# Optimization experiments

Hardware: AMD Instinct MI355X
Metric: run time of the kernel (lower is better)

Reference implementation:

```python
import jax, jax.numpy as jnp
import numpy as np

B, T, C, H = 4, 2048, 1024, 16
D = C // H  # head dim = 64

def setup_inputs() -> dict:
    key = jax.random.key(0)
    k1, k2, k3 = jax.random.split(key, 3)
    y = jax.random.normal(k1, (B, T, C), dtype=jnp.float32)
    W_attn = jax.random.normal(k2, (C, 3 * C), dtype=jnp.float32) * (1.0 / np.sqrt(C))
    b_attn = jnp.zeros((3 * C,), dtype=jnp.float32)
    W_proj = jax.random.normal(k3, (C, C), dtype=jnp.float32) * (1.0 / np.sqrt(C))
    b_proj = jnp.zeros((C,), dtype=jnp.float32)
    return {"y": y, "W_attn": W_attn, "b_attn": b_attn, "W_proj": W_proj, "b_proj": b_proj}

def reference(y, W_attn, b_attn, W_proj, b_proj):
    # qkv projection: [B,T,C] @ [C,3C] -> split into q,k,v
    qkv = y @ W_attn + b_attn
    q, k, v = jnp.split(qkv, 3, axis=-1)
    # [B,T,C] -> [B,H,T,D]
    q = q.reshape(B, T, H, D).swapaxes(1, 2)
    k = k.reshape(B, T, H, D).swapaxes(1, 2)
    v = v.reshape(B, T, H, D).swapaxes(1, 2)
    # scaled dot-product attention, non-causal (config default), dropout=0
    att = jnp.einsum('bhtd,bhrd->bhtr', q, k) * (1.0 / jnp.sqrt(jnp.float32(D)))
    att = jax.nn.softmax(att, axis=-1)
    out = jnp.einsum('bhts,bhsd->bhtd', att, v)
    out = out.swapaxes(1, 2).reshape(B, T, C)
    return out @ W_proj + b_proj
```

## Files before the change

### kernel.cpp

```cpp
#include <hip/hip_runtime.h>
#include <hip/hip_bf16.h>
#include <stdint.h>

#define B_ 4
#define T_ 2048
#define C_ 1024
#define H_ 16
#define D_ 64

typedef short bf16x8 __attribute__((ext_vector_type(8)));
typedef float f32x4 __attribute__((ext_vector_type(4)));
typedef unsigned short u16;

#define QSCALE 0.18033688011112042f

__device__ __forceinline__ u16 f2bf(float f) {
    __hip_bfloat16 h = __float2bfloat16(f);
    return *reinterpret_cast<u16*>(&h);
}

__device__ __forceinline__ float fexp2(float x) {
    float r;
    asm("v_exp_f32 %0, %1" : "=v"(r) : "v"(x));
    return r;
}

__device__ __forceinline__ void gload16(const void* g, void* l) {
    __builtin_amdgcn_global_load_lds(
        (const __attribute__((address_space(1))) unsigned int*)g,
        (__attribute__((address_space(3))) unsigned int*)l, 16, 0, 0);
}

__global__ void k_prep(const float* __restrict__ y, u16* __restrict__ y_bf,
                       const float* __restrict__ Wa, u16* __restrict__ WaT,
                       const float* __restrict__ Wp, u16* __restrict__ WpT) {
    const int bid = blockIdx.x, tid = threadIdx.x;
    if (bid < 8192) {
        int i = (bid * 256 + tid) * 4;
        float4 f = *reinterpret_cast<const float4*>(y + i);
        ushort4 o;
        o.x = f2bf(f.x); o.y = f2bf(f.y); o.z = f2bf(f.z); o.w = f2bf(f.w);
        *reinterpret_cast<ushort4*>(y_bf + i) = o;
        return;
    }
    __shared__ float tile[32][33];
    const float* src; u16* dst; int R, Cc, bx, by;
    if (bid < 8192 + 3072) {
        int idx = bid - 8192;
        src = Wa; dst = WaT; R = 1024; Cc = 3072;
        bx = idx % 96; by = idx / 96;
    } else {
        int idx = bid - 11264;
        src = Wp; dst = WpT; R = 1024; Cc = 1024;
        bx = idx & 31; by = idx >> 5;
    }
    int c0 = bx * 32, r0 = by * 32;
    int tx = tid & 31, ty = tid >> 5;
#pragma unroll
    for (int i = 0; i < 4; i++)
        tile[ty + i * 8][tx] = src[(size_t)(r0 + ty + i * 8) * Cc + c0 + tx];
    __syncthreads();
#pragma unroll
    for (int i = 0; i < 4; i++)
        dst[(size_t)(c0 + ty + i * 8) * R + r0 + tx] = f2bf(tile[tx][ty + i * 8]);
}

template <int EPI>
__launch_bounds__(256, 2)
__global__ void k_gemm(const u16* __restrict__ A, const u16* __restrict__ Bt,
                       const float* __restrict__ bias, int K, int N,
                       float* __restrict__ outf,
                       u16* __restrict__ qw, u16* __restrict__ kw, u16* __restrict__ vw) {
    __shared__ u16 As[128 * 64];
    __shared__ u16 Bs[128 * 64];
    const int tid = threadIdx.x;
    const int lane = tid & 63, w = tid >> 6;
    const int m0 = blockIdx.x * 128, n0 = blockIdx.y * 128;
    const int wm = (w >> 1) * 64, wn = (w & 1) * 64;
    const int lr = lane & 15, lg = lane >> 4;

    f32x4 acc[4][4];
#pragma unroll
    for (int i = 0; i < 4; i++)
#pragma unroll
        for (int j = 0; j < 4; j++) acc[i][j] = (f32x4){0.f, 0.f, 0.f, 0.f};

    const int nk = K >> 6;
    for (int kt = 0; kt < nk; ++kt) {
        const int k0 = kt * 64;
#pragma unroll
        for (int i = 0; i < 4; i++) {
            int c = i * 256 + tid;
            int row = c >> 3, k8 = (c & 7) << 3;
            gload16(A + (size_t)(m0 + row) * K + k0 + k8, (char*)As + i * 4096 + w * 1024);
            gload16(Bt + (size_t)(n0 + row) * K + k0 + k8, (char*)Bs + i * 4096 + w * 1024);
        }
        __syncthreads();
#pragma unroll
        for (int kk = 0; kk < 2; ++kk) {
            bf16x8 af[4], bfr[4];
#pragma unroll
            for (int mf = 0; mf < 4; ++mf)
                af[mf] = *reinterpret_cast<const bf16x8*>(&As[(wm + mf * 16 + lr) * 64 + kk * 32 + lg * 8]);
#pragma unroll
            for (int nf = 0; nf < 4; ++nf)
                bfr[nf] = *reinterpret_cast<const bf16x8*>(&Bs[(wn + nf * 16 + lr) * 64 + kk * 32 + lg * 8]);
#pragma unroll
            for (int mf = 0; mf < 4; ++mf)
#pragma unroll
                for (int nf = 0; nf < 4; ++nf)
                    acc[mf][nf] = __builtin_amdgcn_mfma_f32_16x16x32_bf16(af[mf], bfr[nf], acc[mf][nf], 0, 0, 0);
        }
        __syncthreads();
    }

    if (EPI == 0) {
#pragma unroll
        for (int mf = 0; mf < 4; ++mf)
#pragma unroll
            for (int nf = 0; nf < 4; ++nf) {
                int ng = n0 + wn + nf * 16 + lr;
                float bs = bias[ng];
#pragma unroll
                for (int r = 0; r < 4; ++r) {
                    int mg = m0 + wm + mf * 16 + lg * 4 + r;
                    outf[(size_t)mg * N + ng] = acc[mf][nf][r] + bs;
                }
            }
    } else {
        const int sec = n0 >> 10;
        const float sc = (sec == 0) ? QSCALE : 1.0f;
#pragma unroll
        for (int mf = 0; mf < 4; ++mf)
#pragma unroll
            for (int nf = 0; nf < 4; ++nf) {
                int ng = n0 + wn + nf * 16 + lr;
                float bs = bias[ng];
                int hd = ng & 1023;
                int h = hd >> 6, d = hd & 63;
                int mgb = m0 + wm + mf * 16 + lg * 4;
                int b = mgb >> 11, t0v = mgb & 2047;
                if (sec == 2) {
                    ushort4 pk;
                    pk.x = f2bf(acc[mf][nf][0] + bs);
                    pk.y = f2bf(acc[mf][nf][1] + bs);
                    pk.z = f2bf(acc[mf][nf][2] + bs);
                    pk.w = f2bf(acc[mf][nf][3] + bs);
                    *reinterpret_cast<ushort4*>(&vw[((size_t)(b * H_ + h) * D_ + d) * T_ + t0v]) = pk;
                } else {
                    u16* dst = (sec == 0) ? qw : kw;
#pragma unroll
                    for (int r = 0; r < 4; ++r)
                        dst[((size_t)(b * H_ + h) * T_ + t0v + r) * D_ + d] = f2bf((acc[mf][nf][r] + bs) * sc);
                }
            }
    }
}

__launch_bounds__(128, 2)
__global__ void k_attn(const u16* __restrict__ qw, const u16* __restrict__ kw,
                       const u16* __restrict__ vw, u16* __restrict__ attn) {
    __shared__ u16 Ks[2][64][64];
    __shared__ u16 Vs[2][64][64];
    const int tid = threadIdx.x, lane = tid & 63, w = tid >> 6;
    const int lr = lane & 15, lg = lane >> 4;
    const int bid = blockIdx.x;
    const int logical = (bid & 7) * 128 + (bid >> 3);
    const int bh = logical >> 4, qb = logical & 15;
    const int b = bh >> 4, h = bh & 15;
    const int q0 = qb * 128 + w * 64;
    const u16* qbase = qw + (size_t)bh * T_ * D_;
    const u16* kbase = kw + (size_t)bh * T_ * D_;
    const u16* vbase = vw + (size_t)bh * D_ * T_;

    bf16x8 qf[4][2];
#pragma unroll
    for (int jq = 0; jq < 4; jq++)
#pragma unroll
        for (int kd = 0; kd < 2; kd++)
            qf[jq][kd] = *reinterpret_cast<const bf16x8*>(
                &qbase[(size_t)(q0 + jq * 16 + lr) * D_ + kd * 32 + lg * 8]);

    auto stageK = [&](int kt, int buf) {
#pragma unroll
        for (int i = 0; i < 4; i++) {
            int idx = i * 128 + tid;
            int row = idx >> 3, ch = idx & 7;
            int gch = ch ^ ((row & 3) | (((row >> 3) & 1) << 2));
            gload16(kbase + ((size_t)(kt * 64 + row) * 64 + gch * 8),
                    (char*)&Ks[buf][0][0] + i * 2048 + w * 1024);
        }
    };
    auto stageV = [&](int kt, int buf) {
#pragma unroll
        for (int i = 0; i < 4; i++) {
            int idx = i * 128 + tid;
            int row = idx >> 3, ch = idx & 7;
            int gch = ch ^ (row & 7);
            gload16(vbase + ((size_t)row * T_ + kt * 64 + gch * 8),
                    (char*)&Vs[buf][0][0] + i * 2048 + w * 1024);
        }
    };

    f32x4 o[4][4];
#pragma unroll
    for (int md = 0; md < 4; md++)
#pragma unroll
        for (int jq = 0; jq < 4; jq++) o[md][jq] = (f32x4){0.f, 0.f, 0.f, 0.f};
    float l_run[4] = {0.f, 0.f, 0.f, 0.f};

    const int karow_base = ((lr >> 2) << 3) + (lr & 3);
    const int skl = ((lr & 3) | (((lr >> 2) & 1) << 2)) << 4;

    const int NT = T_ / 64;
    stageK(0, 0);
    stageV(0, 0);

    for (int kt = 0; kt < NT; ++kt) {
        const int cur = kt & 1;
        if (kt + 1 < NT) {
            stageK(kt + 1, cur ^ 1);
            stageV(kt + 1, cur ^ 1);
            asm volatile("s_waitcnt vmcnt(8)" ::: "memory");
        } else {
            asm volatile("s_waitcnt vmcnt(0)" ::: "memory");
        }
        __builtin_amdgcn_s_barrier();

        bf16x8 pfrag[4][2];
#pragma unroll
        for (int g = 0; g < 2; g++) {
            f32x4 st[2][4];
#pragma unroll
            for (int t = 0; t < 2; t++)
#pragma unroll
                for (int jq = 0; jq < 4; jq++) st[t][jq] = (f32x4){0.f, 0.f, 0.f, 0.f};
            __builtin_amdgcn_s_setprio(1);
#pragma unroll
            for (int t = 0; t < 2; t++) {
                int row = g * 32 + karow_base + t * 4;
#pragma unroll
                for (int kd = 0; kd < 2; kd++) {
                    bf16x8 ka = *reinterpret_cast<const bf16x8*>(
                        (const char*)&Ks[cur][0][0] + row * 128 + ((kd * 64 + lg * 16) ^ skl));
#pragma unroll
                    for (int jq = 0; jq < 4; jq++)
                        st[t][jq] = __builtin_amdgcn_mfma_f32_16x16x32_bf16(ka, qf[jq][kd], st[t][jq], 0, 0, 0);
                }
            }
            __builtin_amdgcn_s_setprio(0);
#pragma unroll
            for (int jq = 0; jq < 4; jq++) {
                float p0 = fexp2(st[0][jq][0]), p1 = fexp2(st[0][jq][1]);
                float p2 = fexp2(st[0][jq][2]), p3 = fexp2(st[0][jq][3]);
                float p4 = fexp2(st[1][jq][0]), p5 = fexp2(st[1][jq][1]);
                float p6 = fexp2(st[1][jq][2]), p7 = fexp2(st[1][jq][3]);
                l_run[jq] += ((p0 + p1) + (p2 + p3)) + ((p4 + p5) + (p6 + p7));
                pfrag[jq][g] = (bf16x8){(short)f2bf(p0), (short)f2bf(p1),
                                        (short)f2bf(p2), (short)f2bf(p3),
                                        (short)f2bf(p4), (short)f2bf(p5),
                                        (short)f2bf(p6), (short)f2bf(p7)};
            }
        }

#pragma unroll
        for (int g = 0; g < 2; g++) {
            bf16x8 va[4];
#pragma unroll
            for (int md = 0; md < 4; md++) {
                int row = md * 16 + lr;
                va[md] = *reinterpret_cast<const bf16x8*>(
                    (const char*)&Vs[cur][0][0] + row * 128 + ((g * 64 + lg * 16) ^ ((row & 7) << 4)));
            }
            __builtin_amdgcn_s_setprio(1);
#pragma unroll
            for (int md = 0; md < 4; md++)
#pragma unroll
                for (int jq = 0; jq < 4; jq++)
                    o[md][jq] = __builtin_amdgcn_mfma_f32_16x16x32_bf16(va[md], pfrag[jq][g], o[md][jq], 0, 0, 0);
            __builtin_amdgcn_s_setprio(0);
        }

        __builtin_amdgcn_s_barrier();
    }

#pragma unroll
    for (int jq = 0; jq < 4; jq++) {
        float l = l_run[jq];
        l += __shfl_xor(l, 16);
        l += __shfl_xor(l, 32);
        float rinv = 1.f / l;
        int q = q0 + jq * 16 + lr;
#pragma unroll
        for (int md = 0; md < 4; md++) {
            int d0 = md * 16 + lg * 4;
            ushort4 pk;
            pk.x = f2bf(o[md][jq][0] * rinv);
            pk.y = f2bf(o[md][jq][1] * rinv);
            pk.z = f2bf(o[md][jq][2] * rinv);
            pk.w = f2bf(o[md][jq][3] * rinv);
            *reinterpret_cast<ushort4*>(&attn[((size_t)(b * T_ + q)) * C_ + h * D_ + d0]) = pk;
        }
    }
}

extern "C" void kernel_launch(void* const* d_in, const int* in_sizes, int n_in,
                              void* d_out, int out_size, void* d_ws, size_t ws_size,
                              hipStream_t stream) {
    const float* y = (const float*)d_in[0];
    const float* W_attn = (const float*)d_in[1];
    const float* b_attn = (const float*)d_in[2];
    const float* W_proj = (const float*)d_in[3];
    const float* b_proj = (const float*)d_in[4];

    char* ws = (char*)d_ws;
    u16* y_bf = (u16*)(ws);
    u16* WaT  = (u16*)(ws + 16777216);
    u16* WpT  = (u16*)(ws + 16777216 + 6291456);
    u16* q_ws = (u16*)(ws + 25165824);
    u16* k_ws = (u16*)(ws + 25165824 + 16777216);
    u16* v_ws = (u16*)(ws + 25165824 + 33554432);
    u16* attn = (u16*)(ws + 25165824 + 50331648);

    k_prep<<<12288, 256, 0, stream>>>(y, y_bf, W_attn, WaT, W_proj, WpT);
    k_gemm<1><<<dim3(64, 24), 256, 0, stream>>>(y_bf, WaT, b_attn, 1024, 3072,
                                                nullptr, q_ws, k_ws, v_ws);
    k_attn<<<1024, 128, 0, stream>>>(q_ws, k_ws, v_ws, attn);
    k_gemm<0><<<dim3(64, 8), 256, 0, stream>>>(attn, WpT, b_proj, 1024, 1024,
                                               (float*)d_out, nullptr, nullptr, nullptr);
}
```

Measured before the change: 188.8 us.

## Software-pipeline attention across K tiles with 4 waves and triple-buffered V

Result: slower. 316.8 us (+67.8%).

```diff
diff --git a/kernel.cpp b/kernel.cpp
--- a/kernel.cpp
+++ b/kernel.cpp
@@ -157,135 +157,174 @@
     }
 }
 
-__launch_bounds__(128, 2)
+struct AttnCtx {
+    const char* Kb; const char* Vb;
+    const u16* kbase; const u16* vbase;
+    int tid, w, lr, lg, karow_base, skl;
+};
+
+__device__ __forceinline__ void a_stageK(const AttnCtx& c, int kt, int buf) {
+#pragma unroll
+    for (int i = 0; i < 2; i++) {
+        int idx = i * 256 + c.tid;
+        int row = idx >> 3, ch = idx & 7;
+        int gch = ch ^ ((row & 3) | (((row >> 3) & 1) << 2));
+        gload16(c.kbase + ((size_t)(kt * 64 + row) * 64 + gch * 8),
+                (char*)c.Kb + buf * 8192 + i * 4096 + c.w * 1024);
+    }
+}
+__device__ __forceinline__ void a_stageV(const AttnCtx& c, int kt, int vb) {
+#pragma unroll
+    for (int i = 0; i < 2; i++) {
+        int idx = i * 256 + c.tid;
+        int row = idx >> 3, ch = idx & 7;
+        int gch = ch ^ (row & 7);
+        gload16(c.vbase + ((size_t)row * T_ + kt * 64 + gch * 8),
+                (char*)c.Vb + vb * 8192 + i * 4096 + c.w * 1024);
+    }
+}
+
+template <bool FIRST, bool LAST>
+__device__ __forceinline__ void a_tile(const AttnCtx& c, int t, int curK,
+                                       int vb_cur, int vb_nxt, int vb_old,
+                                       const bf16x8 (&qf)[2][2],
+                                       bf16x8 (&pf_new)[2][2], const bf16x8 (&pf_old)[2][2],
+                                       f32x4 (&o)[4][2], float (&l_run)[2]) {
+    __builtin_amdgcn_s_barrier();
+    if (!LAST) {
+        a_stageK(c, t + 1, curK ^ 1);
+        a_stageV(c, t + 1, vb_nxt);
+        asm volatile("s_waitcnt vmcnt(4)" ::: "memory");
+    } else {
+        asm volatile("s_waitcnt vmcnt(0)" ::: "memory");
+    }
+    __builtin_amdgcn_s_barrier();
+
+    const char* Kc = c.Kb + curK * 8192;
+    const char* Vo = c.Vb + vb_old * 8192;
+#pragma unroll
+    for (int g = 0; g < 2; g++) {
+        f32x4 st[2][2];
+#pragma unroll
+        for (int t2 = 0; t2 < 2; t2++)
+#pragma unroll
+            for (int jq = 0; jq < 2; jq++) st[t2][jq] = (f32x4){0.f, 0.f, 0.f, 0.f};
+        __builtin_amdgcn_s_setprio(1);
+#pragma unroll
+        for (int t2 = 0; t2 < 2; t2++) {
+            int row = g * 32 + c.karow_base + t2 * 4;
+#pragma unroll
+            for (int kd = 0; kd < 2; kd++) {
+                bf16x8 ka = *reinterpret_cast<const bf16x8*>(
+                    Kc + row * 128 + ((kd * 64 + c.lg * 16) ^ c.skl));
+#pragma unroll
+                for (int jq = 0; jq < 2; jq++)
+                    st[t2][jq] = __builtin_amdgcn_mfma_f32_16x16x32_bf16(ka, qf[jq][kd], st[t2][jq], 0, 0, 0);
+            }
+        }
+        if (!FIRST) {
+#pragma unroll
+            for (int md = 0; md < 4; md++) {
+                int row = md * 16 + c.lr;
+                bf16x8 va = *reinterpret_cast<const bf16x8*>(
+                    Vo + row * 128 + ((g * 64 + c.lg * 16) ^ ((row & 7) << 4)));
+#pragma unroll
+                for (int jq = 0; jq < 2; jq++)
+                    o[md][jq] = __builtin_amdgcn_mfma_f32_16x16x32_bf16(va, pf_old[jq][g], o[md][jq], 0, 0, 0);
+            }
+        }
+        __builtin_amdgcn_s_setprio(0);
+#pragma unroll
+        for (int jq = 0; jq < 2; jq++) {
+            float p0 = fexp2(st[0][jq][0]), p1 = fexp2(st[0][jq][1]);
+            float p2 = fexp2(st[0][jq][2]), p3 = fexp2(st[0][jq][3]);
+            float p4 = fexp2(st[1][jq][0]), p5 = fexp2(st[1][jq][1]);
+            float p6 = fexp2(st[1][jq][2]), p7 = fexp2(st[1][jq][3]);
+            l_run[jq] += ((p0 + p1) + (p2 + p3)) + ((p4 + p5) + (p6 + p7));
+            pf_new[jq][g] = (bf16x8){(short)f2bf(p0), (short)f2bf(p1),
+                                     (short)f2bf(p2), (short)f2bf(p3),
+                                     (short)f2bf(p4), (short)f2bf(p5),
+                                     (short)f2bf(p6), (short)f2bf(p7)};
+        }
+    }
+}
+
+__launch_bounds__(256, 4)
 __global__ void k_attn(const u16* __restrict__ qw, const u16* __restrict__ kw,
                        const u16* __restrict__ vw, u16* __restrict__ attn) {
     __shared__ u16 Ks[2][64][64];
-    __shared__ u16 Vs[2][64][64];
+    __shared__ u16 Vs[3][64][64];
     const int tid = threadIdx.x, lane = tid & 63, w = tid >> 6;
     const int lr = lane & 15, lg = lane >> 4;
     const int bid = blockIdx.x;
     const int logical = (bid & 7) * 128 + (bid >> 3);
     const int bh = logical >> 4, qb = logical & 15;
     const int b = bh >> 4, h = bh & 15;
-    const int q0 = qb * 128 + w * 64;
+    const int q0 = qb * 128 + w * 32;
+
+    AttnCtx c;
+    c.Kb = (const char*)&Ks[0][0][0];
+    c.Vb = (const char*)&Vs[0][0][0];
+    c.kbase = kw + (size_t)bh * T_ * D_;
+    c.vbase = vw + (size_t)bh * D_ * T_;
+    c.tid = tid; c.w = w; c.lr = lr; c.lg = lg;
+    c.karow_base = ((lr >> 2) << 3) + (lr & 3);
+    c.skl = ((lr & 3) | (((lr >> 2) & 1) << 2)) << 4;
+
     const u16* qbase = qw + (size_t)bh * T_ * D_;
-    const u16* kbase = kw + (size_t)bh * T_ * D_;
-    const u16* vbase = vw + (size_t)bh * D_ * T_;
-
-    bf16x8 qf[4][2];
-#pragma unroll
-    for (int jq = 0; jq < 4; jq++)
+    bf16x8 qf[2][2];
+#pragma unroll
+    for (int jq = 0; jq < 2; jq++)
 #pragma unroll
         for (int kd = 0; kd < 2; kd++)
             qf[jq][kd] = *reinterpret_cast<const bf16x8*>(
                 &qbase[(size_t)(q0 + jq * 16 + lr) * D_ + kd * 32 + lg * 8]);
 
-    auto stageK = [&](int kt, int buf) {
-#pragma unroll
-        for (int i = 0; i < 4; i++) {
-            int idx = i * 128 + tid;
-            int row = idx >> 3, ch = idx & 7;
-            int gch = ch ^ ((row & 3) | (((row >> 3) & 1) << 2));
-            gload16(kbase + ((size_t)(kt * 64 + row) * 64 + gch * 8),
-                    (char*)&Ks[buf][0][0] + i * 2048 + w * 1024);
-        }
-    };
-    auto stageV = [&](int kt, int buf) {
-#pragma unroll
-        for (int i = 0; i < 4; i++) {
-            int idx = i * 128 + tid;
-            int row = idx >> 3, ch = idx & 7;
-            int gch = ch ^ (row & 7);
-            gload16(vbase + ((size_t)row * T_ + kt * 64 + gch * 8),
-                    (char*)&Vs[buf][0][0] + i * 2048 + w * 1024);
-        }
-    };
-
-    f32x4 o[4][4];
+    f32x4 o[4][2];
 #pragma unroll
     for (int md = 0; md < 4; md++)
 #pragma unroll
-        for (int jq = 0; jq < 4; jq++) o[md][jq] = (f32x4){0.f, 0.f, 0.f, 0.f};
-    float l_run[4] = {0.f, 0.f, 0.f, 0.f};
-
-    const int karow_base = ((lr >> 2) << 3) + (lr & 3);
-    const int skl = ((lr & 3) | (((lr >> 2) & 1) << 2)) << 4;
-
-    const int NT = T_ / 64;
-    stageK(0, 0);
-    stageV(0, 0);
-
-    for (int kt = 0; kt < NT; ++kt) {
-        const int cur = kt & 1;
-        if (kt + 1 < NT) {
-            stageK(kt + 1, cur ^ 1);
-            stageV(kt + 1, cur ^ 1);
-            asm volatile("s_waitcnt vmcnt(8)" ::: "memory");
-        } else {
-            asm volatile("s_waitcnt vmcnt(0)" ::: "memory");
-        }
-        __builtin_amdgcn_s_barrier();
-
-        bf16x8 pfrag[4][2];
-#pragma unroll
-        for (int g = 0; g < 2; g++) {
-            f32x4 st[2][4];
-#pragma unroll
-            for (int t = 0; t < 2; t++)
-#pragma unroll
-                for (int jq = 0; jq < 4; jq++) st[t][jq] = (f32x4){0.f, 0.f, 0.f, 0.f};
-            __builtin_amdgcn_s_setprio(1);
-#pragma unroll
-            for (int t = 0; t < 2; t++) {
-                int row = g * 32 + karow_base + t * 4;
-#pragma unroll
-                for (int kd = 0; kd < 2; kd++) {
-                    bf16x8 ka = *reinterpret_cast<const bf16x8*>(
-                        (const char*)&Ks[cur][0][0] + row * 128 + ((kd * 64 + lg * 16) ^ skl));
-#pragma unroll
-                    for (int jq = 0; jq < 4; jq++)
-                        st[t][jq] = __builtin_amdgcn_mfma_f32_16x16x32_bf16(ka, qf[jq][kd], st[t][jq], 0, 0, 0);
-                }
-            }
-            __builtin_amdgcn_s_setprio(0);
-#pragma unroll
-            for (int jq = 0; jq < 4; jq++) {
-                float p0 = fexp2(st[0][jq][0]), p1 = fexp2(st[0][jq][1]);
-                float p2 = fexp2(st[0][jq][2]), p3 = fexp2(st[0][jq][3]);
-                float p4 = fexp2(st[1][jq][0]), p5 = fexp2(st[1][jq][1]);
-                float p6 = fexp2(st[1][jq][2]), p7 = fexp2(st[1][jq][3]);
-                l_run[jq] += ((p0 + p1) + (p2 + p3)) + ((p4 + p5) + (p6 + p7));
-                pfrag[jq][g] = (bf16x8){(short)f2bf(p0), (short)f2bf(p1),
-                                        (short)f2bf(p2), (short)f2bf(p3),
-                                        (short)f2bf(p4), (short)f2bf(p5),
-                                        (short)f2bf(p6), (short)f2bf(p7)};
-            }
-        }
-
-#pragma unroll
-        for (int g = 0; g < 2; g++) {
-            bf16x8 va[4];
+        for (int jq = 0; jq < 2; jq++) o[md][jq] = (f32x4){0.f, 0.f, 0.f, 0.f};
+    float l_run[2] = {0.f, 0.f};
+    bf16x8 pfA[2][2], pfB[2][2];
+
+    a_stageK(c, 0, 0);
+    a_stageV(c, 0, 0);
+
+    a_tile<true, false>(c, 0, 0, 0, 1, 2, qf, pfA, pfB, o, l_run);
+    a_tile<false, false>(c, 1, 1, 1, 2, 0, qf, pfB, pfA, o, l_run);
+    int v_prev = 1, v_cur = 2;
+    for (int t = 2; t < 30; t += 2) {
+        int v_nxt = (v_cur == 2) ? 0 : v_cur + 1;
+        a_tile<false, false>(c, t, 0, v_cur, v_nxt, v_prev, qf, pfA, pfB, o, l_run);
+        v_prev = v_cur; v_cur = v_nxt; v_nxt = (v_cur == 2) ? 0 : v_cur + 1;
+        a_tile<false, false>(c, t + 1, 1, v_cur, v_nxt, v_prev, qf, pfB, pfA, o, l_run);
+        v_prev = v_cur; v_cur = v_nxt;
+    }
+    {
+        int v_nxt = (v_cur == 2) ? 0 : v_cur + 1;
+        a_tile<false, false>(c, 30, 0, v_cur, v_nxt, v_prev, qf, pfA, pfB, o, l_run);
+        v_prev = v_cur; v_cur = v_nxt;
+    }
+    a_tile<false, true>(c, 31, 1, v_cur, 0, v_prev, qf, pfB, pfA, o, l_run);
+
+    {
+        const char* Vf = c.Vb + v_cur * 8192;
+#pragma unroll
+        for (int g = 0; g < 2; g++)
 #pragma unroll
             for (int md = 0; md < 4; md++) {
                 int row = md * 16 + lr;
-                va[md] = *reinterpret_cast<const bf16x8*>(
-                    (const char*)&Vs[cur][0][0] + row * 128 + ((g * 64 + lg * 16) ^ ((row & 7) << 4)));
-            }
-            __builtin_amdgcn_s_setprio(1);
-#pragma unroll
-            for (int md = 0; md < 4; md++)
-#pragma unroll
-                for (int jq = 0; jq < 4; jq++)
-                    o[md][jq] = __builtin_amdgcn_mfma_f32_16x16x32_bf16(va[md], pfrag[jq][g], o[md][jq], 0, 0, 0);
-            __builtin_amdgcn_s_setprio(0);
-        }
-
-        __builtin_amdgcn_s_barrier();
-    }
-
-#pragma unroll
-    for (int jq = 0; jq < 4; jq++) {
+                bf16x8 va = *reinterpret_cast<const bf16x8*>(
+                    Vf + row * 128 + ((g * 64 + lg * 16) ^ ((row & 7) << 4)));
+#pragma unroll
+                for (int jq = 0; jq < 2; jq++)
+                    o[md][jq] = __builtin_amdgcn_mfma_f32_16x16x32_bf16(va, pfB[jq][g], o[md][jq], 0, 0, 0);
+            }
+    }
+
+#pragma unroll
+    for (int jq = 0; jq < 2; jq++) {
         float l = l_run[jq];
         l += __shfl_xor(l, 16);
         l += __shfl_xor(l, 32);
@@ -325,7 +364,7 @@
     k_prep<<<12288, 256, 0, stream>>>(y, y_bf, W_attn, WaT, W_proj, WpT);
     k_gemm<1><<<dim3(64, 24), 256, 0, stream>>>(y_bf, WaT, b_attn, 1024, 3072,
                                                 nullptr, q_ws, k_ws, v_ws);
-    k_attn<<<1024, 128, 0, stream>>>(q_ws, k_ws, v_ws, attn);
+    k_attn<<<1024, 256, 0, stream>>>(q_ws, k_ws, v_ws, attn);
     k_gemm<0><<<dim3(64, 8), 256, 0, stream>>>(attn, WpT, b_proj, 1024, 1024,
                                                (float*)d_out, nullptr, nullptr, nullptr);
 }
```
